# Optimization experiments

Hardware: AMD Instinct MI355X
Metric: run time of the kernel (lower is better)

Reference implementation:

```python
import jax, jax.numpy as jnp
import numpy as np

B, T, IN, H, NC = 128, 256, 512, 1024, 10


def setup_inputs() -> dict:
    key = jax.random.key(0)
    ks = jax.random.split(key, 18)
    s = jnp.float32(0.05)

    def n(k, shape):
        return jax.random.normal(k, shape, dtype=jnp.float32) * s

    inp = {"x": n(ks[0], (B, T, IN))}
    in_dims = [IN, H, H]
    ki = 1
    for l in range(3):
        inp[f"w_ih{l}"] = n(ks[ki], (4 * H, in_dims[l])); ki += 1
        inp[f"w_hh{l}"] = n(ks[ki], (4 * H, H)); ki += 1
        inp[f"b_ih{l}"] = n(ks[ki], (4 * H,)); ki += 1
        inp[f"b_hh{l}"] = n(ks[ki], (4 * H,)); ki += 1
    inp["w1"] = n(ks[ki], (32, H)); ki += 1
    inp["b1"] = n(ks[ki], (32,)); ki += 1
    inp["w2"] = n(ks[ki], (NC, 32)); ki += 1
    inp["b2"] = n(ks[ki], (NC,))
    return inp


def _lstm_layer(xs, w_ih, w_hh, b):
    # xs: [B, T, D_in]; PyTorch gate order i, f, g, o
    bsz = xs.shape[0]
    hid = w_hh.shape[1]
    # Precompute input projection for all timesteps (one big GEMM)
    xp = jnp.einsum('bti,gi->btg', xs, w_ih) + b  # [B, T, 4H]

    def step(carry, xp_t):
        h, c = carry
        gates = xp_t + h @ w_hh.T  # [B, 4H]
        i, f, g, o = jnp.split(gates, 4, axis=-1)
        c = jax.nn.sigmoid(f) * c + jax.nn.sigmoid(i) * jnp.tanh(g)
        h = jax.nn.sigmoid(o) * jnp.tanh(c)
        return (h, c), h

    h0 = jnp.zeros((bsz, hid), xs.dtype)
    c0 = jnp.zeros((bsz, hid), xs.dtype)
    (_, _), hs = jax.lax.scan(step, (h0, c0), jnp.swapaxes(xp, 0, 1))
    return jnp.swapaxes(hs, 0, 1)  # [B, T, H]


def reference(x, w_ih0, w_hh0, b_ih0, b_hh0,
              w_ih1, w_hh1, b_ih1, b_hh1,
              w_ih2, w_hh2, b_ih2, b_hh2,
              w1, b1, w2, b2):
    h = x
    layers = [(w_ih0, w_hh0, b_ih0, b_hh0),
              (w_ih1, w_hh1, b_ih1, b_hh1),
              (w_ih2, w_hh2, b_ih2, b_hh2)]
    for w_ih, w_hh, b_ih, b_hh in layers:
        h = _lstm_layer(h, w_ih, w_hh, b_ih + b_hh)
    last = h[:, -1, :]                      # [B, H]
    hid = jax.nn.relu(last @ w1.T + b1)     # [B, 32]
    return hid @ w2.T + b2                  # [B, NC]
```

## Files before the change

kernel.cpp:

```cpp
#include <hip/hip_runtime.h>
#include <hip/hip_bf16.h>
#include <stdint.h>

#define B_ 128
#define T_ 256
#define IN_ 512
#define H_ 1024
#define G4_ 4096
#define TC_ 64
#define NCHUNK_ (T_ / TC_)

typedef __bf16 bf16x8 __attribute__((ext_vector_type(8)));
typedef float f32x4 __attribute__((ext_vector_type(4)));

#define AS1U(p) ((const __attribute__((address_space(1))) unsigned int*)(p))
#define AS3U(p) ((__attribute__((address_space(3))) unsigned int*)(p))

__device__ __forceinline__ uint16_t f2bf(float f) {
  union { float f; uint32_t u; } v; v.f = f;
  uint32_t r = (v.u + 0x7fffu + ((v.u >> 16) & 1u)) >> 16;
  return (uint16_t)r;
}
__device__ __forceinline__ float bf2f(uint16_t h) {
  union { uint32_t u; float f; } v; v.u = ((uint32_t)h) << 16;
  return v.f;
}
__device__ __forceinline__ float sigmoid_f(float x) {
  return 1.f / (1.f + __expf(-x));
}
__device__ __forceinline__ float tanh_f(float x) {
  x = fminf(15.f, fmaxf(-15.f, x));
  float e = __expf(2.f * x);
  return (e - 1.f) / (e + 1.f);
}

__global__ void k_f32_to_bf16(const float* __restrict__ src, uint16_t* __restrict__ dst, int n) {
  int i = (blockIdx.x * blockDim.x + threadIdx.x) * 4;
  if (i >= n) return;
  float4 v = *(const float4*)(src + i);
  ushort4 o;
  o.x = f2bf(v.x); o.y = f2bf(v.y); o.z = f2bf(v.z); o.w = f2bf(v.w);
  *(ushort4*)(dst + i) = o;
}

__global__ void k_bias(const float* __restrict__ a, const float* __restrict__ b, float* __restrict__ o) {
  int i = blockIdx.x * blockDim.x + threadIdx.x;
  if (i < G4_) o[i] = a[i] + b[i];
}

__global__ void k_whh_frag(const float* __restrict__ whh, uint16_t* __restrict__ dst) {
  int t = blockIdx.x * blockDim.x + threadIdx.x;
  int lane = t & 63;
  int kk = (t >> 6) & 15;
  int w  = (t >> 10) & 15;
  int s5 = t >> 14;
  int nt = w & 7, kh = w >> 3;
  int row = (nt >> 1) * 1024 + s5 * 32 + (nt & 1) * 16 + (lane & 15);
  int col = kh * 512 + kk * 32 + ((lane >> 4) << 3);
  const float* sp = whh + (size_t)row * H_ + col;
  uint16_t o[8];
  #pragma unroll
  for (int j = 0; j < 8; ++j) o[j] = f2bf(sp[j]);
  uint4 pk;
  __builtin_memcpy(&pk, o, 16);
  *(uint4*)(dst + (size_t)t * 8) = pk;
}

__global__ __launch_bounds__(256, 1) void k_gemm_xp(
    const uint16_t* __restrict__ A, const uint16_t* __restrict__ W,
    const float* __restrict__ bias, uint16_t* __restrict__ xp,
    int K, int t0)
{
  __shared__ __align__(16) uint16_t As[128 * 32];
  __shared__ __align__(16) uint16_t Bs[128 * 32];
  __shared__ __align__(16) uint16_t Cs[128][136];
  const int tid = threadIdx.x;
  const int l = tid & 63;
  const int w = tid >> 6;
  const int mx = blockIdx.x;
  const int n0 = blockIdx.y * 128;
  const int wm = (w >> 1) * 64;
  const int wn = (w & 1) * 64;

  f32x4 acc[4][4] = {};

  for (int k0 = 0; k0 < K; k0 += 32) {
    __syncthreads();
    #pragma unroll
    for (int it = 0; it < 2; ++it) {
      const int chunk = w * 2 + it;
      const int loff = chunk * 1024 + l * 16;
      const int row = loff >> 6;
      const int colb = loff & 63;
      const int gm = mx * 512 + t0 + ((row >> 6) << 8) + (row & 63);
      const uint16_t* ga = A + (size_t)gm * K + k0 + (colb >> 1);
      __builtin_amdgcn_global_load_lds(AS1U(ga), AS3U((char*)As + chunk * 1024), 16, 0, 0);
      const uint16_t* gb = W + (size_t)(n0 + row) * K + k0 + (colb >> 1);
      __builtin_amdgcn_global_load_lds(AS1U(gb), AS3U((char*)Bs + chunk * 1024), 16, 0, 0);
    }
    __syncthreads();
    bf16x8 af[4], bfr[4];
    #pragma unroll
    for (int i = 0; i < 4; ++i)
      af[i] = *(const bf16x8*)&As[(wm + i * 16 + (l & 15)) * 32 + ((l >> 4) << 3)];
    #pragma unroll
    for (int j = 0; j < 4; ++j)
      bfr[j] = *(const bf16x8*)&Bs[(wn + j * 16 + (l & 15)) * 32 + ((l >> 4) << 3)];
    #pragma unroll
    for (int i = 0; i < 4; ++i) {
      #pragma unroll
      for (int j = 0; j < 4; ++j)
        acc[i][j] = __builtin_amdgcn_mfma_f32_16x16x32_bf16(af[i], bfr[j], acc[i][j], 0, 0, 0);
    }
  }

  #pragma unroll
  for (int i = 0; i < 4; ++i) {
    const int row = wm + i * 16 + ((l >> 4) << 2);
    #pragma unroll
    for (int j = 0; j < 4; ++j) {
      const int col = wn + j * 16 + (l & 15);
      const float bv = bias[n0 + col];
      #pragma unroll
      for (int r = 0; r < 4; ++r)
        Cs[row + r][col] = f2bf(acc[i][j][r] + bv);
    }
  }
  __syncthreads();
  #pragma unroll
  for (int it = 0; it < 8; ++it) {
    const int row = it * 16 + w * 4 + (l >> 4);
    uint4 v = *(const uint4*)&Cs[row][(l & 15) * 8];
    *(uint4*)(xp + (size_t)(mx * 128 + row) * G4_ + n0 + (l & 15) * 8) = v;
  }
}

__global__ __launch_bounds__(1024, 4) void k_lstm(
    const uint16_t* __restrict__ whhf, const uint16_t* __restrict__ xp,
    uint16_t* __restrict__ seq, uint32_t* __restrict__ hbuf,
    float* __restrict__ cbuf, unsigned int* __restrict__ flags, int t0, int sall)
{
  __shared__ __align__(16) uint16_t Astg[2048 * 8];
  __shared__ float part[2][8][16][17];
  const int tid = threadIdx.x;
  const int l = tid & 63;
  const int w = tid >> 6;
  const int nt = w & 7;
  const int kh = w >> 3;
  const int bid = blockIdx.x;
  const int g = bid & 7;
  const int s5 = bid >> 3;
  const int U0 = s5 * 32;
  const int gs0 = g * 16;

  unsigned int* gflag = flags + g * 32;

  bf16x8 bfr[16];
  {
    const uint16_t* wp = whhf + (size_t)(s5 * 16 + w) * 8192 + l * 8;
    #pragma unroll
    for (int kk = 0; kk < 16; ++kk)
      bfr[kk] = *(const bf16x8*)(wp + kk * 512);
  }

  const int u = tid & 31;
  const int smg = (tid >> 5) & 15;
  float cc = 0.f;
  if (tid < 512) cc = cbuf[(size_t)(gs0 + smg) * H_ + U0 + u];

  uint16_t x0 = 0, x1 = 0, x2 = 0, x3 = 0;
  if (tid < 512) {
    const uint16_t* p = xp + ((size_t)(gs0 + smg) * TC_ + 0) * G4_ + U0 + u;
    x0 = p[0]; x1 = p[1024]; x2 = p[2048]; x3 = p[3072];
  }

  auto stage_h = [&](int par) {
    const char* src = (const char*)hbuf + (size_t)par * (B_ * H_ * 2)
                      + (size_t)(gs0 + w) * 2048 + (size_t)l * 32;
    const uint64_t* s8 = (const uint64_t*)src;
    uint64_t a = __hip_atomic_load(s8 + 0, __ATOMIC_RELAXED, __HIP_MEMORY_SCOPE_SYSTEM);
    uint64_t b = __hip_atomic_load(s8 + 1, __ATOMIC_RELAXED, __HIP_MEMORY_SCOPE_SYSTEM);
    uint64_t c = __hip_atomic_load(s8 + 2, __ATOMIC_RELAXED, __HIP_MEMORY_SCOPE_SYSTEM);
    uint64_t d = __hip_atomic_load(s8 + 3, __ATOMIC_RELAXED, __HIP_MEMORY_SCOPE_SYSTEM);
    const int base = 512 * l + ((w ^ (l & 7)) << 4);
    uint64_t* d0 = (uint64_t*)((char*)Astg + base);
    d0[0] = a; d0[1] = b;
    uint64_t* d1 = (uint64_t*)((char*)Astg + base + 256);
    d1[0] = c; d1[1] = d;
  };

  stage_h(0);
  __syncthreads();

  for (int tl = 0; tl < TC_; ++tl) {
    const int par = tl & 1;

    f32x4 e0 = {0.f, 0.f, 0.f, 0.f};
    f32x4 e1 = {0.f, 0.f, 0.f, 0.f};
    #pragma unroll
    for (int kk = 0; kk < 16; kk += 2) {
      const int c0 = kh * 64 + kk * 4 + (l >> 4);
      const int c1 = c0 + 4;
      const int sw0 = (l & 15) ^ ((2 * kk + (l >> 5)) & 7);
      const int sw1 = (l & 15) ^ ((2 * (kk + 1) + (l >> 5)) & 7);
      bf16x8 a0 = *(const bf16x8*)((const char*)Astg + (c0 << 8) + (sw0 << 4));
      bf16x8 a1 = *(const bf16x8*)((const char*)Astg + (c1 << 8) + (sw1 << 4));
      e0 = __builtin_amdgcn_mfma_f32_16x16x32_bf16(a0, bfr[kk],     e0, 0, 0, 0);
      e1 = __builtin_amdgcn_mfma_f32_16x16x32_bf16(a1, bfr[kk + 1], e1, 0, 0, 0);
    }
    f32x4 e = e0 + e1;
    #pragma unroll
    for (int r = 0; r < 4; ++r)
      part[kh][nt][((l >> 4) << 2) + r][l & 15] = e[r];
    __syncthreads();

    if (tid < 512) {
      const int sub = u >> 4, uc = u & 15;
      float gi = part[0][0 + sub][smg][uc] + part[1][0 + sub][smg][uc] + bf2f(x0);
      float gf = part[0][2 + sub][smg][uc] + part[1][2 + sub][smg][uc] + bf2f(x1);
      float gg = part[0][4 + sub][smg][uc] + part[1][4 + sub][smg][uc] + bf2f(x2);
      float go = part[0][6 + sub][smg][uc] + part[1][6 + sub][smg][uc] + bf2f(x3);
      cc = sigmoid_f(gf) * cc + sigmoid_f(gi) * tanh_f(gg);
      float hh = sigmoid_f(go) * tanh_f(cc);
      uint16_t hb = f2bf(hh);
      if (tl + 1 < TC_) {
        const uint16_t* p = xp + ((size_t)(gs0 + smg) * TC_ + tl + 1) * G4_ + U0 + u;
        x0 = p[0]; x1 = p[1024]; x2 = p[2048]; x3 = p[3072];
      }
      unsigned int o = (unsigned int)__shfl_xor((int)(unsigned int)hb, 1);
      if ((u & 1) == 0) {
        uint32_t pk = (uint32_t)hb | (o << 16);
        const int b = gs0 + smg;
        uint32_t* hp = hbuf + (size_t)(1 - par) * (B_ * H_ / 2)
                            + ((size_t)b * H_ + U0 + u) / 2;
        __hip_atomic_store(hp, pk, __ATOMIC_RELAXED, __HIP_MEMORY_SCOPE_SYSTEM);
        if (sall || (t0 + tl == T_ - 1)) {
          uint32_t* sq = (uint32_t*)seq + (((size_t)b * T_ + (t0 + tl)) * H_ + U0 + u) / 2;
          *sq = pk;
        }
      }
    }
    __syncthreads();
    if (tid == 0)
      __hip_atomic_store(gflag + s5, (unsigned)(tl + 1),
                         __ATOMIC_RELAXED, __HIP_MEMORY_SCOPE_SYSTEM);
    if (tid < 32) {
      const unsigned tgt = (unsigned)(tl + 1);
      while (__hip_atomic_load(gflag + tid, __ATOMIC_RELAXED,
                               __HIP_MEMORY_SCOPE_SYSTEM) < tgt)
        __builtin_amdgcn_s_sleep(1);
    }
    __syncthreads();
    if (tl + 1 < TC_) {
      stage_h((tl + 1) & 1);
      __syncthreads();
    }
  }
  if (tid < 512) cbuf[(size_t)(gs0 + smg) * H_ + U0 + u] = cc;
}

__global__ __launch_bounds__(256) void k_mlp(
    const uint16_t* __restrict__ seq2,
    const float* __restrict__ w1, const float* __restrict__ b1,
    const float* __restrict__ w2, const float* __restrict__ b2,
    float* __restrict__ out)
{
  __shared__ float hv[H_];
  __shared__ float part[32][8];
  __shared__ float hid[32];
  const int b = blockIdx.x, tid = threadIdx.x;
  const uint16_t* hrow = seq2 + ((size_t)b * T_ + (T_ - 1)) * H_;
  for (int i = tid; i < H_; i += 256) hv[i] = bf2f(hrow[i]);
  __syncthreads();
  const int j = tid >> 3, p = tid & 7;
  float sum = 0.f;
  const float* wr = w1 + (size_t)j * H_ + p * 128;
  const float* hp = hv + p * 128;
  for (int k = 0; k < 128; ++k) sum += wr[k] * hp[k];
  part[j][p] = sum;
  __syncthreads();
  if (tid < 32) {
    float s2 = 0.f;
    #pragma unroll
    for (int pp = 0; pp < 8; ++pp) s2 += part[tid][pp];
    hid[tid] = fmaxf(s2 + b1[tid], 0.f);
  }
  __syncthreads();
  if (tid < 10) {
    float o = b2[tid];
    #pragma unroll
    for (int jj = 0; jj < 32; ++jj) o += hid[jj] * w2[tid * 32 + jj];
    out[b * 10 + tid] = o;
  }
}

extern "C" void kernel_launch(void* const* d_in, const int* in_sizes, int n_in,
                              void* d_out, int out_size, void* d_ws, size_t ws_size,
                              hipStream_t stream)
{
  const float* x = (const float*)d_in[0];
  const float* w_ih[3] = {(const float*)d_in[1], (const float*)d_in[5], (const float*)d_in[9]};
  const float* w_hh[3] = {(const float*)d_in[2], (const float*)d_in[6], (const float*)d_in[10]};
  const float* b_ih[3] = {(const float*)d_in[3], (const float*)d_in[7], (const float*)d_in[11]};
  const float* b_hh[3] = {(const float*)d_in[4], (const float*)d_in[8], (const float*)d_in[12]};
  const float* w1 = (const float*)d_in[13];
  const float* b1 = (const float*)d_in[14];
  const float* w2 = (const float*)d_in[15];
  const float* b2 = (const float*)d_in[16];
  float* out = (float*)d_out;

  char* ws = (char*)d_ws;
  size_t off = 0;
  auto alloc = [&](size_t bytes) {
    char* p = ws + off;
    off += (bytes + 255) & ~(size_t)255;
    return p;
  };
  uint16_t* XBF  = (uint16_t*)alloc((size_t)B_ * T_ * IN_ * 2);
  uint16_t* WIH0 = (uint16_t*)alloc((size_t)G4_ * IN_ * 2);
  uint16_t* WIH1 = (uint16_t*)alloc((size_t)G4_ * H_ * 2);
  uint16_t* WIH2 = (uint16_t*)alloc((size_t)G4_ * H_ * 2);
  float*    BIAS = (float*)alloc((size_t)3 * G4_ * 4);
  uint16_t* WHHF = (uint16_t*)alloc((size_t)3 * G4_ * H_ * 2);
  uint16_t* XP   = (uint16_t*)alloc((size_t)B_ * TC_ * G4_ * 2);
  uint16_t* SEQ  = (uint16_t*)alloc((size_t)B_ * T_ * H_ * 2);
  uint32_t* HBUF = (uint32_t*)alloc((size_t)2 * B_ * H_ * 2);
  float*    CBUF = (float*)alloc((size_t)B_ * H_ * 4);
  unsigned int* FLG = (unsigned int*)alloc((size_t)3 * NCHUNK_ * 1024 * 4);

  hipMemsetAsync(FLG, 0, (size_t)3 * NCHUNK_ * 1024 * 4, stream);

  int n;
  n = B_ * T_ * IN_;
  k_f32_to_bf16<<<n / 4 / 256, 256, 0, stream>>>(x, XBF, n);
  n = G4_ * IN_;
  k_f32_to_bf16<<<n / 4 / 256, 256, 0, stream>>>(w_ih[0], WIH0, n);
  n = G4_ * H_;
  k_f32_to_bf16<<<n / 4 / 256, 256, 0, stream>>>(w_ih[1], WIH1, n);
  k_f32_to_bf16<<<n / 4 / 256, 256, 0, stream>>>(w_ih[2], WIH2, n);
  for (int li = 0; li < 3; ++li)
    k_bias<<<16, 256, 0, stream>>>(b_ih[li], b_hh[li], BIAS + li * G4_);
  for (int li = 0; li < 3; ++li)
    k_whh_frag<<<2048, 256, 0, stream>>>(w_hh[li], WHHF + (size_t)li * G4_ * H_);

  const uint16_t* seq_in[3] = {XBF, SEQ, SEQ};
  const uint16_t* wih[3] = {WIH0, WIH1, WIH2};
  const int Ks[3] = {IN_, H_, H_};

  for (int li = 0; li < 3; ++li) {
    hipMemsetAsync(HBUF, 0, (size_t)2 * B_ * H_ * 2, stream);
    hipMemsetAsync(CBUF, 0, (size_t)B_ * H_ * 4, stream);
    const int sall = (li == 2) ? 0 : 1;
    for (int c = 0; c < NCHUNK_; ++c) {
      dim3 grid(64, 32);
      k_gemm_xp<<<grid, 256, 0, stream>>>(seq_in[li], wih[li], BIAS + li * G4_, XP,
                                          Ks[li], c * TC_);
      unsigned int* flg_lc = FLG + (size_t)(li * NCHUNK_ + c) * 1024;
      k_lstm<<<256, 1024, 0, stream>>>(WHHF + (size_t)li * G4_ * H_, XP, SEQ, HBUF,
                                       CBUF, flg_lc, c * TC_, sall);
    }
  }
  k_mlp<<<B_, 256, 0, stream>>>(SEQ, w1, b1, w2, b2, out);
}
```

Baseline: 3.999 ms.

## Fuse cross-block flag polling with h-state loads to drop a barrier per step

After: 3.329 ms. 16.8% less time.

```diff
diff --git a/kernel.cpp b/kernel.cpp
--- a/kernel.cpp
+++ b/kernel.cpp
@@ -12,6 +12,7 @@
 
 typedef __bf16 bf16x8 __attribute__((ext_vector_type(8)));
 typedef float f32x4 __attribute__((ext_vector_type(4)));
+typedef uint32_t u32x4 __attribute__((ext_vector_type(4)));
 
 #define AS1U(p) ((const __attribute__((address_space(1))) unsigned int*)(p))
 #define AS3U(p) ((__attribute__((address_space(3))) unsigned int*)(p))
@@ -174,22 +175,32 @@
     x0 = p[0]; x1 = p[1024]; x2 = p[2048]; x3 = p[3072];
   }
 
-  auto stage_h = [&](int par) {
+  auto stage_fused = [&](int tl) {
+    const int par = tl & 1;
+    const unsigned tgt = (unsigned)tl;
     const char* src = (const char*)hbuf + (size_t)par * (B_ * H_ * 2)
                       + (size_t)(gs0 + w) * 2048 + (size_t)l * 32;
-    const uint64_t* s8 = (const uint64_t*)src;
-    uint64_t a = __hip_atomic_load(s8 + 0, __ATOMIC_RELAXED, __HIP_MEMORY_SCOPE_SYSTEM);
-    uint64_t b = __hip_atomic_load(s8 + 1, __ATOMIC_RELAXED, __HIP_MEMORY_SCOPE_SYSTEM);
-    uint64_t c = __hip_atomic_load(s8 + 2, __ATOMIC_RELAXED, __HIP_MEMORY_SCOPE_SYSTEM);
-    uint64_t d = __hip_atomic_load(s8 + 3, __ATOMIC_RELAXED, __HIP_MEMORY_SCOPE_SYSTEM);
+    const unsigned int* fp = gflag + (l >> 1);
+    u32x4 q0, q1;
+    unsigned fv;
+    do {
+      asm volatile(
+        "global_load_dword %0, %3, off sc0 sc1\n\t"
+        "global_load_dwordx4 %1, %4, off sc0 sc1\n\t"
+        "global_load_dwordx4 %2, %4, off offset:16 sc0 sc1\n\t"
+        "s_waitcnt vmcnt(0)"
+        : "=&v"(fv), "=&v"(q0), "=&v"(q1)
+        : "v"(fp), "v"(src)
+        : "memory");
+      if (fv >= tgt) break;
+      __builtin_amdgcn_s_sleep(1);
+    } while (true);
     const int base = 512 * l + ((w ^ (l & 7)) << 4);
-    uint64_t* d0 = (uint64_t*)((char*)Astg + base);
-    d0[0] = a; d0[1] = b;
-    uint64_t* d1 = (uint64_t*)((char*)Astg + base + 256);
-    d1[0] = c; d1[1] = d;
+    *(u32x4*)((char*)Astg + base) = q0;
+    *(u32x4*)((char*)Astg + base + 256) = q1;
   };
 
-  stage_h(0);
+  stage_fused(0);
   __syncthreads();
 
   for (int tl = 0; tl < TC_; ++tl) {
@@ -223,10 +234,6 @@
       cc = sigmoid_f(gf) * cc + sigmoid_f(gi) * tanh_f(gg);
       float hh = sigmoid_f(go) * tanh_f(cc);
       uint16_t hb = f2bf(hh);
-      if (tl + 1 < TC_) {
-        const uint16_t* p = xp + ((size_t)(gs0 + smg) * TC_ + tl + 1) * G4_ + U0 + u;
-        x0 = p[0]; x1 = p[1024]; x2 = p[2048]; x3 = p[3072];
-      }
       unsigned int o = (unsigned int)__shfl_xor((int)(unsigned int)hb, 1);
       if ((u & 1) == 0) {
         uint32_t pk = (uint32_t)hb | (o << 16);
@@ -239,20 +246,17 @@
           *sq = pk;
         }
       }
+      if (tl + 1 < TC_) {
+        const uint16_t* p = xp + ((size_t)(gs0 + smg) * TC_ + tl + 1) * G4_ + U0 + u;
+        x0 = p[0]; x1 = p[1024]; x2 = p[2048]; x3 = p[3072];
+      }
     }
     __syncthreads();
     if (tid == 0)
       __hip_atomic_store(gflag + s5, (unsigned)(tl + 1),
                          __ATOMIC_RELAXED, __HIP_MEMORY_SCOPE_SYSTEM);
-    if (tid < 32) {
-      const unsigned tgt = (unsigned)(tl + 1);
-      while (__hip_atomic_load(gflag + tid, __ATOMIC_RELAXED,
-                               __HIP_MEMORY_SCOPE_SYSTEM) < tgt)
-        __builtin_amdgcn_s_sleep(1);
-    }
-    __syncthreads();
     if (tl + 1 < TC_) {
-      stage_h((tl + 1) & 1);
+      stage_fused(tl + 1);
       __syncthreads();
     }
   }
```
